# Performance work log

Measured on AMD Instinct MI355X. Metric: run time of the kernel, lower is better.

The kernel has to match this reference:

```python
import jax, jax.numpy as jnp
import numpy as np


def setup_inputs() -> dict:
    key = jax.random.key(0)
    ks = jax.random.split(key, 5)
    B, NINS, NHID = 128, 4096, 128
    inputs = jax.random.normal(ks[0], (B, NINS, NHID), dtype=jnp.float32)
    claims = jax.random.normal(ks[1], (B, NHID), dtype=jnp.float32)  # unused by forward
    # project: Linear(2*nhid -> 64) -> ReLU -> Linear(64 -> 1)
    W1 = jax.random.normal(ks[2], (2 * NHID, 64), dtype=jnp.float32) * (1.0 / np.sqrt(2 * NHID))
    b1 = jnp.zeros((64,), dtype=jnp.float32)
    W2 = jax.random.normal(ks[3], (64, 1), dtype=jnp.float32) * (1.0 / np.sqrt(64))
    b2 = jnp.zeros((1,), dtype=jnp.float32)
    return {"inputs": inputs, "index": 5, "claims": claims,
            "W1": W1, "b1": b1, "W2": W2, "b2": b2}


def reference(inputs, index, claims, W1, b1, W2, b2):
    # inputs: [B, nins, nhid]
    B, NINS, NHID = inputs.shape
    own = jax.lax.dynamic_slice_in_dim(inputs, index, 1, axis=1)  # [B, 1, nhid]
    own = jnp.broadcast_to(own, (B, NINS, NHID))                  # repeat over nins
    tmp = jnp.concatenate([own, inputs], axis=2)                  # [B, nins, 2*nhid]
    h = jax.nn.relu(jnp.einsum('bnd,dk->bnk', tmp, W1) + b1)      # [B, nins, 64]
    att = jnp.einsum('bnk,ko->bno', h, W2) + b2                   # [B, nins, 1]
    weights = jax.nn.softmax(att[..., 0], axis=1)                 # [B, nins]
    outputs = jnp.einsum('bnd,bn->bd', inputs, weights)           # [B, nhid]
    return outputs
```

## Files before the change

kernel.cpp:

```cpp
#include <hip/hip_runtime.h>
#include <math.h>

#define BATCH 128
#define NINS  4096
#define NHID  128
#define KH    64
#define NPART 128
#define PART_STRIDE 136
#define O_OFF 8
#define TPW 2

typedef __attribute__((ext_vector_type(8))) short short8;
typedef __attribute__((ext_vector_type(4))) float f32x4;

__device__ inline unsigned short f2bf(float f) {
    union { float f; unsigned u; } v; v.f = f;
    return (unsigned short)((v.u + 0x7FFFu + ((v.u >> 16) & 1u)) >> 16);
}

__device__ inline unsigned cvt_pk_u32(float a, float b) {
#if __has_builtin(__builtin_amdgcn_cvt_pk_bf16_f32)
    typedef __attribute__((ext_vector_type(2))) __bf16 bf16x2;
    bf16x2 p = __builtin_amdgcn_cvt_pk_bf16_f32(a, b);
    unsigned u; __builtin_memcpy(&u, &p, 4); return u;
#else
    return (unsigned)f2bf(a) | ((unsigned)f2bf(b) << 16);
#endif
}

__device__ inline void cvt2(short8& f, int j, float a, float b) {
    unsigned u = cvt_pk_u32(a, b);
    f[j] = (short)(u & 0xffffu); f[j + 1] = (short)(u >> 16);
}

__global__ void precompute_c(const float* __restrict__ inputs,
                             const int* __restrict__ index_p,
                             const float* __restrict__ W1,
                             const float* __restrict__ b1,
                             float* __restrict__ c) {
    const int b = blockIdx.x;
    const int k = threadIdx.x;
    const int idx = index_p[0];
    const float* own = inputs + ((size_t)b * NINS + idx) * NHID;
    float acc = b1[k];
    #pragma unroll 8
    for (int d = 0; d < NHID; ++d)
        acc = fmaf(own[d], W1[d * KH + k], acc);
    c[b * KH + k] = acc;
}

__global__ __launch_bounds__(256, 4)
void att_partial(const float* __restrict__ inputs,
                 const float* __restrict__ W1,
                 const float* __restrict__ W2,
                 const float* __restrict__ b2_p,
                 const float* __restrict__ c,
                 float* __restrict__ part) {
    __shared__ unsigned short WbT[KH][NHID + 8];
    __shared__ float ebuf[4][32];

    const int tid  = threadIdx.x;
    const int lane = tid & 63;
    const int wv   = tid >> 6;
    const int b    = blockIdx.y;
    const int quad = lane >> 4;
    const int m16  = lane & 15;

    const float* xb = inputs + (size_t)b * NINS * NHID;

    {
        const int n  = tid >> 2;
        const int kb = (tid & 3) * 32;
        const float* wp = W1 + (size_t)(NHID + kb) * KH + n;
        #pragma unroll
        for (int j = 0; j < 32; j += 2) {
            unsigned u = cvt_pk_u32(wp[(size_t)j * KH], wp[(size_t)(j + 1) * KH]);
            *(unsigned*)&WbT[n][kb + j] = u;
        }
    }
    __syncthreads();

    float w2v[4];
    #pragma unroll
    for (int nf = 0; nf < 4; ++nf) w2v[nf] = W2[nf * 16 + m16];
    const float b2v = b2_p[0];
    float cv[4];
    #pragma unroll
    for (int nf = 0; nf < 4; ++nf) cv[nf] = c[b * KH + nf * 16 + m16];

    for (int t = 0; t < TPW; ++t) {
        const int tile = (blockIdx.x * 4 + wv) * TPW + t;
        const int n0   = tile * 32;

        f32x4 acc[2][4];
        #pragma unroll
        for (int mf = 0; mf < 2; ++mf)
            #pragma unroll
            for (int nf = 0; nf < 4; ++nf) {
                f32x4 z = {cv[nf], cv[nf], cv[nf], cv[nf]};
                acc[mf][nf] = z;
            }

        #pragma unroll
        for (int ks = 0; ks < 4; ++ks) {
            short8 Bf[4];
            #pragma unroll
            for (int nf = 0; nf < 4; ++nf)
                Bf[nf] = *(const short8*)&WbT[nf * 16 + m16][ks * 32 + quad * 8];

            short8 Af[2];
            #pragma unroll
            for (int mf = 0; mf < 2; ++mf) {
                const float* row = xb + (size_t)(n0 + mf * 16 + m16) * NHID
                                      + ks * 32 + quad * 8;
                f32x4 a  = *(const f32x4*)row;
                f32x4 bq = *(const f32x4*)(row + 4);
                short8 f;
                cvt2(f, 0, a.x,  a.y);
                cvt2(f, 2, a.z,  a.w);
                cvt2(f, 4, bq.x, bq.y);
                cvt2(f, 6, bq.z, bq.w);
                Af[mf] = f;
            }
            #pragma unroll
            for (int mf = 0; mf < 2; ++mf)
                #pragma unroll
                for (int nf = 0; nf < 4; ++nf)
                    acc[mf][nf] = __builtin_amdgcn_mfma_f32_16x16x32_bf16(
                        Af[mf], Bf[nf], acc[mf][nf], 0, 0, 0);
        }

        float att[2][4];
        #pragma unroll
        for (int mf = 0; mf < 2; ++mf)
            #pragma unroll
            for (int r = 0; r < 4; ++r) {
                float s = 0.0f;
                #pragma unroll
                for (int nf = 0; nf < 4; ++nf)
                    s = fmaf(fmaxf(acc[mf][nf][r], 0.0f), w2v[nf], s);
                s += __shfl_xor(s, 1);
                s += __shfl_xor(s, 2);
                s += __shfl_xor(s, 4);
                s += __shfl_xor(s, 8);
                att[mf][r] = s + b2v;
            }

        float mx = att[0][0];
        #pragma unroll
        for (int mf = 0; mf < 2; ++mf)
            #pragma unroll
            for (int r = 0; r < 4; ++r) mx = fmaxf(mx, att[mf][r]);
        mx = fmaxf(mx, __shfl_xor(mx, 16));
        mx = fmaxf(mx, __shfl_xor(mx, 32));

        float ev[2][4];
        float L = 0.0f;
        #pragma unroll
        for (int mf = 0; mf < 2; ++mf)
            #pragma unroll
            for (int r = 0; r < 4; ++r) {
                ev[mf][r] = __expf(att[mf][r] - mx);
                L += ev[mf][r];
            }
        L += __shfl_xor(L, 16);
        L += __shfl_xor(L, 32);

        if (m16 == 0) {
            #pragma unroll
            for (int mf = 0; mf < 2; ++mf)
                #pragma unroll
                for (int r = 0; r < 4; ++r)
                    ebuf[wv][mf * 16 + quad * 4 + r] = ev[mf][r];
        }

        const int G  = lane >> 5;
        const int db = (lane & 31) * 4;
        f32x4 e4[4];
        #pragma unroll
        for (int i = 0; i < 4; ++i)
            e4[i] = *(const f32x4*)&ebuf[wv][G * 16 + i * 4];

        f32x4 o = {0.0f, 0.0f, 0.0f, 0.0f};
        const float* xr = xb + (size_t)(n0 + G * 16) * NHID + db;
        #pragma unroll
        for (int jj = 0; jj < 16; ++jj) {
            f32x4 xv = *(const f32x4*)(xr + (size_t)jj * NHID);
            o += xv * e4[jj >> 2][jj & 3];
        }
        #pragma unroll
        for (int i = 0; i < 4; ++i) o[i] += __shfl_xor(o[i], 32);

        float* p = part + (size_t)(b * NPART + tile) * PART_STRIDE;
        if (lane == 0) { p[0] = mx; p[1] = L; }
        if (lane < 32) *(f32x4*)(p + O_OFF + db) = o;
    }
}

__global__ void finalize(const float* __restrict__ part,
                         float* __restrict__ out) {
    const int b = blockIdx.x;
    const int d = threadIdx.x;
    const float* pb = part + (size_t)b * NPART * PART_STRIDE;

    float M = pb[0];
    #pragma unroll 8
    for (int p = 1; p < NPART; ++p)
        M = fmaxf(M, pb[p * PART_STRIDE]);

    float S = 0.0f, acc = 0.0f;
    #pragma unroll 4
    for (int p = 0; p < NPART; ++p) {
        const float sc = __expf(pb[p * PART_STRIDE] - M);
        S   = fmaf(sc, pb[p * PART_STRIDE + 1], S);
        acc = fmaf(sc, pb[p * PART_STRIDE + O_OFF + d], acc);
    }
    out[b * NHID + d] = acc / S;
}

extern "C" void kernel_launch(void* const* d_in, const int* in_sizes, int n_in,
                              void* d_out, int out_size, void* d_ws, size_t ws_size,
                              hipStream_t stream) {
    const float* inputs = (const float*)d_in[0];
    const int*   index  = (const int*)  d_in[1];
    const float* W1     = (const float*)d_in[3];
    const float* b1     = (const float*)d_in[4];
    const float* W2     = (const float*)d_in[5];
    const float* b2     = (const float*)d_in[6];
    float* out = (float*)d_out;

    float* c    = (float*)d_ws;
    float* part = c + BATCH * KH;

    precompute_c<<<dim3(BATCH), dim3(64), 0, stream>>>(inputs, index, W1, b1, c);

    dim3 gB(NPART / (4 * TPW), BATCH);
    att_partial<<<gB, dim3(256), 0, stream>>>(inputs, W1, W2, b2, c, part);

    finalize<<<dim3(BATCH), dim3(NHID), 0, stream>>>(part, out);
}
```

Baseline: 417.7 us.

## Stage input tiles into LDS as bf16 with coalesced loads and prefetch

Each wave now loads its 32-row input tile with fully coalesced 16-byte loads, converts it to bf16 and writes it into a padded per-wave shared-memory buffer. The MFMA A fragments are then read from LDS rather than through strided per-lane global loads. The next tile is staged while the current one is computed. The extra LDS (about 34 KB) lowers the launch-bounds occupancy target from 4 to 3 blocks. The second pass over x for the weighted sum still reads global memory (likely hitting cache).

```diff
diff --git a/kernel.cpp b/kernel.cpp
--- a/kernel.cpp
+++ b/kernel.cpp
@@ -9,6 +9,7 @@
 #define PART_STRIDE 136
 #define O_OFF 8
 #define TPW 2
+#define XP 136
 
 typedef __attribute__((ext_vector_type(8))) short short8;
 typedef __attribute__((ext_vector_type(4))) float f32x4;
@@ -26,11 +27,6 @@
 #else
     return (unsigned)f2bf(a) | ((unsigned)f2bf(b) << 16);
 #endif
-}
-
-__device__ inline void cvt2(short8& f, int j, float a, float b) {
-    unsigned u = cvt_pk_u32(a, b);
-    f[j] = (short)(u & 0xffffu); f[j + 1] = (short)(u >> 16);
 }
 
 __global__ void precompute_c(const float* __restrict__ inputs,
@@ -49,14 +45,15 @@
     c[b * KH + k] = acc;
 }
 
-__global__ __launch_bounds__(256, 4)
+__global__ __launch_bounds__(256, 3)
 void att_partial(const float* __restrict__ inputs,
                  const float* __restrict__ W1,
                  const float* __restrict__ W2,
                  const float* __restrict__ b2_p,
                  const float* __restrict__ c,
                  float* __restrict__ part) {
-    __shared__ unsigned short WbT[KH][NHID + 8];
+    __shared__ unsigned short WbT[KH][XP];
+    __shared__ unsigned short Xs[4][32][XP];
     __shared__ float ebuf[4][32];
 
     const int tid  = threadIdx.x;
@@ -88,9 +85,36 @@
     #pragma unroll
     for (int nf = 0; nf < 4; ++nf) cv[nf] = c[b * KH + nf * 16 + m16];
 
+    const int base = (blockIdx.x * 4 + wv) * TPW;
+
+    auto stage = [&](int n0) {
+        const float* src = xb + (size_t)n0 * NHID;
+        unsigned short* xw = &Xs[wv][0][0];
+        #pragma unroll
+        for (int i = 0; i < 16; ++i) {
+            const int f = i * 64 + lane;
+            f32x4 v = *(const f32x4*)(src + (size_t)f * 4);
+            uint2 u;
+            u.x = cvt_pk_u32(v.x, v.y);
+            u.y = cvt_pk_u32(v.z, v.w);
+            *(uint2*)(xw + (f >> 5) * XP + (f & 31) * 4) = u;
+        }
+    };
+
+    stage(base * 32);
+
     for (int t = 0; t < TPW; ++t) {
-        const int tile = (blockIdx.x * 4 + wv) * TPW + t;
+        const int tile = base + t;
         const int n0   = tile * 32;
+
+        short8 Af[2][4];
+        #pragma unroll
+        for (int mf = 0; mf < 2; ++mf)
+            #pragma unroll
+            for (int ks = 0; ks < 4; ++ks)
+                Af[mf][ks] = *(const short8*)&Xs[wv][mf * 16 + m16][ks * 32 + quad * 8];
+
+        if (t + 1 < TPW) stage((tile + 1) * 32);
 
         f32x4 acc[2][4];
         #pragma unroll
@@ -107,27 +131,12 @@
             #pragma unroll
             for (int nf = 0; nf < 4; ++nf)
                 Bf[nf] = *(const short8*)&WbT[nf * 16 + m16][ks * 32 + quad * 8];
-
-            short8 Af[2];
-            #pragma unroll
-            for (int mf = 0; mf < 2; ++mf) {
-                const float* row = xb + (size_t)(n0 + mf * 16 + m16) * NHID
-                                      + ks * 32 + quad * 8;
-                f32x4 a  = *(const f32x4*)row;
-                f32x4 bq = *(const f32x4*)(row + 4);
-                short8 f;
-                cvt2(f, 0, a.x,  a.y);
-                cvt2(f, 2, a.z,  a.w);
-                cvt2(f, 4, bq.x, bq.y);
-                cvt2(f, 6, bq.z, bq.w);
-                Af[mf] = f;
-            }
             #pragma unroll
             for (int mf = 0; mf < 2; ++mf)
                 #pragma unroll
                 for (int nf = 0; nf < 4; ++nf)
                     acc[mf][nf] = __builtin_amdgcn_mfma_f32_16x16x32_bf16(
-                        Af[mf], Bf[nf], acc[mf][nf], 0, 0, 0);
+                        Af[mf][ks], Bf[nf], acc[mf][nf], 0, 0, 0);
         }
 
         float att[2][4];
```

New measurement: 413.1 us. Within noise of the previous version (-1.1%).
